# Performance work log

Hardware: AMD Instinct MI355X
Metric: run time of the kernel (lower is better)

The kernel has to match this reference:

```python
import jax, jax.numpy as jnp
import numpy as np

GAMMA = 0.1


def spmm(edge_index, edge_weight, feat, n_nodes):
    # y[dst] += w * feat[src]  -- sparse adjacency @ feat via gather/scatter
    src = edge_index[0]
    dst = edge_index[1]
    msgs = feat[src] * edge_weight[:, None]  # [E, d]
    return jax.ops.segment_sum(msgs, dst, num_segments=n_nodes)


def setup_inputs() -> dict:
    key = jax.random.key(0)
    ks = jax.random.split(key, 12)
    N, F, H, O = 50000, 500, 64, 16
    E, Ek = 1600000, 1000000
    x = jax.random.normal(ks[0], (N, F), dtype=jnp.float32)
    edge_index = jax.random.randint(ks[1], (2, E), 0, N, dtype=jnp.int32)
    edge_weight = jax.random.uniform(ks[2], (E,), dtype=jnp.float32)
    knn_edge_index = jax.random.randint(ks[3], (2, Ek), 0, N, dtype=jnp.int32)
    knn_edge_weight = jax.random.uniform(ks[4], (Ek,), dtype=jnp.float32)
    # glorot-ish scaled params
    W0 = jax.random.normal(ks[5], (F, H), dtype=jnp.float32) * (1.0 / np.sqrt(F))
    W1 = jax.random.normal(ks[6], (H, O), dtype=jnp.float32) * (1.0 / np.sqrt(H))
    score0 = jax.random.normal(ks[7], (F, 1), dtype=jnp.float32) * (1.0 / np.sqrt(F))
    score1 = jax.random.normal(ks[8], (H, 1), dtype=jnp.float32) * (1.0 / np.sqrt(H))
    Dk0 = jax.random.normal(ks[9], (F, 1), dtype=jnp.float32) * (1.0 / np.sqrt(F))
    Dk1 = jax.random.normal(ks[10], (H, 1), dtype=jnp.float32) * (1.0 / np.sqrt(H))
    z = jnp.zeros((1,), dtype=jnp.float32)
    return {
        "x": x, "edge_index": edge_index, "edge_weight": edge_weight,
        "knn_edge_index": knn_edge_index, "knn_edge_weight": knn_edge_weight,
        "W0": W0, "W1": W1,
        "score0": score0, "sbias0": z, "score1": score1, "sbias1": z,
        "Dk0": Dk0, "Dbias0": z, "Dk1": Dk1, "Dbias1": z,
    }


def reference(x, edge_index, edge_weight, knn_edge_index, knn_edge_weight,
              W0, W1, score0, sbias0, score1, sbias1,
              Dk0, Dbias0, Dk1, Dbias1):
    N = x.shape[0]
    layers = [(W0, score0, sbias0, Dk0, Dbias0),
              (W1, score1, sbias1, Dk1, Dbias1)]
    for W, sc, sb, dkw, dkb in layers:
        s = jax.nn.sigmoid(x @ sc + sb)          # [N, 1] gate
        Dk = x @ dkw + dkb                        # [N, 1] degree-like scale
        xW = x @ W                                # shared linear transform
        agg = spmm(edge_index, edge_weight, xW, N)        # GCNConv(x, adj)
        agg_knn = spmm(knn_edge_index, knn_edge_weight, xW, N)  # GCNConv(x, adj_knn)
        # acts are identity (acts=[None] and final act None); dropout off (eval)
        x = s * agg + (1.0 - s) * agg_knn + GAMMA * Dk * xW
    return x
```

## Files before the change

### kernel.cpp

```cpp
#include <hip/hip_runtime.h>
#include <math.h>

#define GAMMA 0.1f

typedef float f32x4 __attribute__((ext_vector_type(4)));
typedef short short4v __attribute__((ext_vector_type(4)));
typedef short short8 __attribute__((ext_vector_type(8)));

static __device__ __forceinline__ unsigned short f2bf(float f) {
  union { float f; unsigned u; } v; v.f = f;
  unsigned r = v.u + 0x7FFF + ((v.u >> 16) & 1);
  return (unsigned short)(r >> 16);
}
static __device__ __forceinline__ float bf2f(unsigned short b) {
  union { unsigned u; float f; } v; v.u = ((unsigned)b) << 16;
  return v.f;
}

__global__ __launch_bounds__(256) void build_bt3(
    const float* __restrict__ W, const float* __restrict__ sc,
    const float* __restrict__ dk, unsigned short* __restrict__ Bt3,
    int H, int Kact, int KPAD, int COLS) {
  int i = blockIdx.x * 256 + threadIdx.x;
  if (i >= COLS * KPAD) return;
  int c = i / KPAD;
  int k = i - c * KPAD;
  float v = 0.f;
  if (k < Kact) {
    if (c < H) v = W[(size_t)k * H + c];
    else if (c == H) v = sc[k];
    else if (c == H + 1) v = dk[k];
  }
  Bt3[(size_t)((k >> 3) * COLS + c) * 8 + (k & 7)] = f2bf(v);
}

__global__ __launch_bounds__(256) void zero_cnt(int* __restrict__ p, int n) {
  int i = blockIdx.x * 256 + threadIdx.x;
  if (i < n) p[i] = 0;
}

template <int CFRAGS, int OUTFRAGS, int COLS>
__global__ __launch_bounds__(256) void mfma_linear_l0(
    const float* __restrict__ A, const unsigned short* __restrict__ Bt3,
    const float* __restrict__ sb, const float* __restrict__ db,
    unsigned short* __restrict__ outW, float* __restrict__ s,
    float* __restrict__ Dk, int N, int Kact) {
  constexpr int KPAD = 512;
  constexpr int KSPLIT = 4, RPB = 16;
  constexpr int KS_PER = (KPAD / 32) / KSPLIT;
  constexpr int H = OUTFRAGS * 16;
  __shared__ unsigned short Ald[RPB * KPAD];
  __shared__ float red[(KSPLIT - 1) * 64 * CFRAGS * 4];

  const int t = threadIdx.x;
  const int rowBase = blockIdx.x * RPB;

#pragma unroll
  for (int it = 0; it < (RPB * KPAD) / (256 * 4); ++it) {
    int li = it * 1024 + t * 4;
    int row = li >> 9;
    int col = li & 511;
    int grow = rowBase + row;
    f32x4 v = (f32x4)0.f;
    if (grow < N && col < Kact)
      v = *(const f32x4*)(A + (size_t)grow * Kact + col);
    short4v b;
#pragma unroll
    for (int j = 0; j < 4; ++j) b[j] = (short)f2bf(v[j]);
    int byte = row * (KPAD * 2) + ((col * 2) ^ ((row & 7) << 4));
    *(short4v*)((char*)Ald + byte) = b;
  }
  __syncthreads();

  const int kslice = t >> 6;
  const int l = t & 63;
  const int kgrp = l >> 4;
  const int lc = l & 15;
  const int lrow = lc;
  const int rowD = rowBase + kgrp * 4;

  f32x4 acc[CFRAGS];
#pragma unroll
  for (int i = 0; i < CFRAGS; ++i) acc[i] = (f32x4)0.f;

  const int rbyte = lrow * (KPAD * 2);
  const int rswz = (lrow & 7) << 4;
#pragma unroll
  for (int kk = 0; kk < KS_PER; ++kk) {
    const int ks = kslice * KS_PER + kk;
    short8 av = *(const short8*)((char*)Ald +
                                 (rbyte + ((ks * 64 + kgrp * 16) ^ rswz)));
    const unsigned short* bbase =
        Bt3 + (size_t)((ks * 4 + kgrp) * COLS + lc) * 8;
#pragma unroll
    for (int fc = 0; fc < CFRAGS; ++fc) {
      short8 bv = *(const short8*)(bbase + fc * 128);
      acc[fc] = __builtin_amdgcn_mfma_f32_16x16x32_bf16(av, bv, acc[fc], 0, 0, 0);
    }
  }

  if (kslice > 0) {
    float* dst = red + ((kslice - 1) * 64 + l) * (CFRAGS * 4);
#pragma unroll
    for (int fc = 0; fc < CFRAGS; ++fc)
#pragma unroll
      for (int r = 0; r < 4; ++r) dst[fc * 4 + r] = acc[fc][r];
  }
  __syncthreads();
  if (kslice == 0) {
#pragma unroll
    for (int s2 = 1; s2 < KSPLIT; ++s2) {
      const float* src2 = red + ((s2 - 1) * 64 + l) * (CFRAGS * 4);
#pragma unroll
      for (int fc = 0; fc < CFRAGS; ++fc)
#pragma unroll
        for (int r = 0; r < 4; ++r) acc[fc][r] += src2[fc * 4 + r];
    }
#pragma unroll
    for (int fc = 0; fc < OUTFRAGS; ++fc) {
#pragma unroll
      for (int r = 0; r < 4; ++r) {
        int gr = rowD + r;
        if (gr < N) outW[(size_t)gr * H + fc * 16 + lc] = f2bf(acc[fc][r]);
      }
    }
    if (lc < 2) {
      f32x4 g = acc[CFRAGS - 1];
#pragma unroll
      for (int r = 0; r < 4; ++r) {
        int gr = rowD + r;
        if (gr < N) {
          if (lc == 0) s[gr] = 1.f / (1.f + expf(-(g[r] + sb[0])));
          else Dk[gr] = g[r] + db[0];
        }
      }
    }
  }
}

template <int KPAD, int CFRAGS, int OUTFRAGS, int COLS>
__global__ __launch_bounds__(256) void mfma_linear_bf(
    const unsigned short* __restrict__ Aptr, const unsigned short* __restrict__ Bt3,
    const float* __restrict__ sb, const float* __restrict__ db,
    unsigned short* __restrict__ outW, float* __restrict__ s,
    float* __restrict__ Dk, int N, int Kact) {
  constexpr int H = OUTFRAGS * 16;
  constexpr int KSPLIT = 2, RG = 2, RPB = 32;
  constexpr int KS_PER = (KPAD / 32) / KSPLIT;
  __shared__ float red[(KSPLIT - 1) * RG * 64 * CFRAGS * 4];

  const int w = threadIdx.x >> 6;
  const int rowgrp = w % RG;
  const int kslice = w / RG;
  const int l = threadIdx.x & 63;
  const int kgrp = l >> 4;
  const int lc = l & 15;
  const int rowA = blockIdx.x * RPB + rowgrp * 16 + lc;
  const int rowD = blockIdx.x * RPB + rowgrp * 16 + kgrp * 4;
  const int rowSafe = (rowA < N) ? rowA : 0;

  f32x4 acc[CFRAGS];
#pragma unroll
  for (int i = 0; i < CFRAGS; ++i) acc[i] = (f32x4)0.f;

#pragma unroll
  for (int kk = 0; kk < KS_PER; ++kk) {
    const int ks = kslice * KS_PER + kk;
    const int kb = ks * 32 + kgrp * 8;
    short8 av = *(const short8*)(Aptr + (size_t)rowSafe * Kact + kb);
    const unsigned short* bbase =
        Bt3 + (size_t)((ks * 4 + kgrp) * COLS + lc) * 8;
#pragma unroll
    for (int fc = 0; fc < CFRAGS; ++fc) {
      short8 bv = *(const short8*)(bbase + fc * 128);
      acc[fc] = __builtin_amdgcn_mfma_f32_16x16x32_bf16(av, bv, acc[fc], 0, 0, 0);
    }
  }

  if (kslice > 0) {
    float* dst = red + ((rowgrp)*64 + l) * (CFRAGS * 4);
#pragma unroll
    for (int fc = 0; fc < CFRAGS; ++fc)
#pragma unroll
      for (int r = 0; r < 4; ++r) dst[fc * 4 + r] = acc[fc][r];
  }
  __syncthreads();
  if (kslice == 0) {
    const float* src2 = red + ((rowgrp)*64 + l) * (CFRAGS * 4);
#pragma unroll
    for (int fc = 0; fc < CFRAGS; ++fc)
#pragma unroll
      for (int r = 0; r < 4; ++r) acc[fc][r] += src2[fc * 4 + r];

#pragma unroll
    for (int fc = 0; fc < OUTFRAGS; ++fc) {
#pragma unroll
      for (int r = 0; r < 4; ++r) {
        int gr = rowD + r;
        if (gr < N) outW[(size_t)gr * H + fc * 16 + lc] = f2bf(acc[fc][r]);
      }
    }
    if (lc < 2) {
      f32x4 g = acc[CFRAGS - 1];
#pragma unroll
      for (int r = 0; r < 4; ++r) {
        int gr = rowD + r;
        if (gr < N) {
          if (lc == 0) s[gr] = 1.f / (1.f + expf(-(g[r] + sb[0])));
          else Dk[gr] = g[r] + db[0];
        }
      }
    }
  }
}

#define BIN_CHUNK 8192

__global__ __launch_bounds__(512) void bucket_count2(
    const int* __restrict__ eiA, int EA, int* __restrict__ bcntA,
    const int* __restrict__ eiK, int EK, int* __restrict__ bcntK, int nchA) {
  const int* ei;
  int E, chunk;
  int* bcnt;
  if (blockIdx.x < nchA) { ei = eiA; E = EA; bcnt = bcntA; chunk = blockIdx.x; }
  else { ei = eiK; E = EK; bcnt = bcntK; chunk = blockIdx.x - nchA; }
  __shared__ int lc[256];
  if (threadIdx.x < 256) lc[threadIdx.x] = 0;
  __syncthreads();
  const int base = chunk * BIN_CHUNK;
  for (int k = threadIdx.x; k < BIN_CHUNK; k += 512) {
    int e = base + k;
    if (e < E) atomicAdd(&lc[ei[E + e] >> 8], 1);
  }
  __syncthreads();
  if (threadIdx.x < 256 && lc[threadIdx.x])
    atomicAdd(&bcnt[threadIdx.x], lc[threadIdx.x]);
}

__global__ __launch_bounds__(512) void bucket_scan2(
    int* __restrict__ bcntA, int* __restrict__ boffA, int* __restrict__ gcurA,
    int* __restrict__ bcntK, int* __restrict__ boffK, int* __restrict__ gcurK,
    int nb) {
  int* bcnt = blockIdx.x ? bcntK : bcntA;
  int* boff = blockIdx.x ? boffK : boffA;
  int* gcur = blockIdx.x ? gcurK : gcurA;
  __shared__ int sh[512];
  int t = threadIdx.x;
  int v = (t < nb) ? bcnt[t] : 0;
  sh[t] = v;
  __syncthreads();
  int acc = v;
  for (int off = 1; off < 512; off <<= 1) {
    int xx = (t >= off) ? sh[t - off] : 0;
    __syncthreads();
    acc += xx;
    sh[t] = acc;
    __syncthreads();
  }
  if (t < nb) {
    boff[t] = acc - v;
    gcur[t] = acc - v;
  }
  if (t == nb - 1) boff[nb] = acc;
}

__global__ __launch_bounds__(512) void bin_fill2(
    const int* __restrict__ eiA, const float* __restrict__ ewA, int EA,
    int* __restrict__ gcurA, int2* __restrict__ recA,
    const int* __restrict__ eiK, const float* __restrict__ ewK, int EK,
    int* __restrict__ gcurK, int2* __restrict__ recK, int nchA) {
  const int* ei;
  const float* ew;
  int E, chunk;
  int* gcur;
  int2* rec;
  if (blockIdx.x < nchA) {
    ei = eiA; ew = ewA; E = EA; gcur = gcurA; rec = recA; chunk = blockIdx.x;
  } else {
    ei = eiK; ew = ewK; E = EK; gcur = gcurK; rec = recK;
    chunk = blockIdx.x - nchA;
  }
  __shared__ int scnt[256];
  __shared__ int scur[256];
  if (threadIdx.x < 256) scnt[threadIdx.x] = 0;
  __syncthreads();
  const int base = chunk * BIN_CHUNK;
  for (int k = threadIdx.x; k < BIN_CHUNK; k += 512) {
    int e = base + k;
    if (e < E) atomicAdd(&scnt[ei[E + e] >> 8], 1);
  }
  __syncthreads();
  if (threadIdx.x < 256 && scnt[threadIdx.x])
    scur[threadIdx.x] = atomicAdd(&gcur[threadIdx.x], scnt[threadIdx.x]);
  __syncthreads();
  for (int k = threadIdx.x; k < BIN_CHUNK; k += 512) {
    int e = base + k;
    if (e < E) {
      int src = ei[e];
      int dst = ei[E + e];
      int pos = atomicAdd(&scur[dst >> 8], 1);
      rec[pos] = make_int2(((dst & 255) << 16) | src, __float_as_int(ew[e]));
    }
  }
}

__global__ __launch_bounds__(512) void tile_sort2(
    const int2* __restrict__ recRawA, const int* __restrict__ boffA,
    unsigned* __restrict__ recSA, int* __restrict__ rpA,
    const int2* __restrict__ recRawK, const int* __restrict__ boffK,
    unsigned* __restrict__ recSK, int* __restrict__ rpK, int N, int nb) {
  const int2* recRaw;
  const int* boff;
  unsigned* recS;
  int* rp;
  int tile;
  if (blockIdx.x < nb) {
    recRaw = recRawA; boff = boffA; recS = recSA; rp = rpA; tile = blockIdx.x;
  } else {
    recRaw = recRawK; boff = boffK; recS = recSK; rp = rpK;
    tile = blockIdx.x - nb;
  }
  __shared__ int cnt[256];
  __shared__ int sc[256];
  __shared__ int cur[256];
  const int lo = boff[tile], hi = boff[tile + 1];
  const int t = threadIdx.x;
  if (t < 256) cnt[t] = 0;
  __syncthreads();
  for (int j = lo + t; j < hi; j += 512)
    atomicAdd(&cnt[recRaw[j].x >> 16], 1);
  __syncthreads();
  if (t < 256) sc[t] = cnt[t];
  __syncthreads();
  for (int off = 1; off < 256; off <<= 1) {
    int v = 0;
    if (t < 256 && t >= off) v = sc[t - off];
    __syncthreads();
    if (t < 256) sc[t] += v;
    __syncthreads();
  }
  if (t < 256) {
    int excl = sc[t] - cnt[t];
    cur[t] = excl;
    int n = tile * 256 + t;
    if (n < N) rp[n] = lo + excl;
  }
  if (tile == nb - 1 && t == 0) rp[N] = hi;
  __syncthreads();
  for (int j = lo + t; j < hi; j += 512) {
    int2 r = recRaw[j];
    int pos = lo + atomicAdd(&cur[r.x >> 16], 1);
    recS[pos] = ((unsigned)f2bf(__int_as_float(r.y)) << 16) |
                (unsigned)(r.x & 0xFFFF);
  }
}

static __device__ __forceinline__ float gather64(
    const int* __restrict__ rp, const unsigned* __restrict__ rec,
    const unsigned short* __restrict__ feat, int n, int h) {
  int b = rp[n], e = rp[n + 1];
  float a[16];
#pragma unroll
  for (int u = 0; u < 16; ++u) a[u] = 0.f;
  int j = b;
  for (; j + 16 <= e; j += 16) {
#pragma unroll
    for (int u = 0; u < 16; ++u) {
      unsigned r = rec[j + u];
      a[u] += bf2f((unsigned short)(r >> 16)) *
              bf2f(feat[(size_t)(r & 0xFFFF) * 64 + h]);
    }
  }
  for (; j + 4 <= e; j += 4) {
#pragma unroll
    for (int u = 0; u < 4; ++u) {
      unsigned r = rec[j + u];
      a[u] += bf2f((unsigned short)(r >> 16)) *
              bf2f(feat[(size_t)(r & 0xFFFF) * 64 + h]);
    }
  }
  for (; j < e; ++j) {
    unsigned r = rec[j];
    a[0] += bf2f((unsigned short)(r >> 16)) *
            bf2f(feat[(size_t)(r & 0xFFFF) * 64 + h]);
  }
  float t0 = ((a[0] + a[1]) + (a[2] + a[3])) + ((a[4] + a[5]) + (a[6] + a[7]));
  float t1 = ((a[8] + a[9]) + (a[10] + a[11])) +
             ((a[12] + a[13]) + (a[14] + a[15]));
  return t0 + t1;
}

__global__ __launch_bounds__(256) void agg_combine64(
    const int* __restrict__ rpA, const unsigned* __restrict__ recA,
    const int* __restrict__ rpK, const unsigned* __restrict__ recK,
    const unsigned short* __restrict__ feat, const float* __restrict__ s,
    const float* __restrict__ Dk, unsigned short* __restrict__ outp, int N) {
  int n = __builtin_amdgcn_readfirstlane((blockIdx.x * 256 + threadIdx.x) >> 6);
  if (n >= N) return;
  int h = threadIdx.x & 63;
  float aA = gather64(rpA, recA, feat, n, h);
  float aK = gather64(rpK, recK, feat, n, h);
  float sv = s[n];
  float res = sv * aA + (1.f - sv) * aK +
              GAMMA * Dk[n] * bf2f(feat[(size_t)n * 64 + h]);
  outp[(size_t)n * 64 + h] = f2bf(res);
}

static __device__ __forceinline__ float gather16(
    const int* __restrict__ rp, const unsigned* __restrict__ rec,
    const unsigned short* __restrict__ feat, int n, int h) {
  int b = rp[n], e = rp[n + 1];
  float a0 = 0.f, a1 = 0.f, a2 = 0.f, a3 = 0.f;
  float a4 = 0.f, a5 = 0.f, a6 = 0.f, a7 = 0.f;
  int j = b;
  for (; j + 8 <= e; j += 8) {
    unsigned q0 = rec[j + 0];
    unsigned q1 = rec[j + 1];
    unsigned q2 = rec[j + 2];
    unsigned q3 = rec[j + 3];
    unsigned q4 = rec[j + 4];
    unsigned q5 = rec[j + 5];
    unsigned q6 = rec[j + 6];
    unsigned q7 = rec[j + 7];
    a0 += bf2f((unsigned short)(q0 >> 16)) *
          bf2f(feat[(size_t)(q0 & 0xFFFF) * 16 + h]);
    a1 += bf2f((unsigned short)(q1 >> 16)) *
          bf2f(feat[(size_t)(q1 & 0xFFFF) * 16 + h]);
    a2 += bf2f((unsigned short)(q2 >> 16)) *
          bf2f(feat[(size_t)(q2 & 0xFFFF) * 16 + h]);
    a3 += bf2f((unsigned short)(q3 >> 16)) *
          bf2f(feat[(size_t)(q3 & 0xFFFF) * 16 + h]);
    a4 += bf2f((unsigned short)(q4 >> 16)) *
          bf2f(feat[(size_t)(q4 & 0xFFFF) * 16 + h]);
    a5 += bf2f((unsigned short)(q5 >> 16)) *
          bf2f(feat[(size_t)(q5 & 0xFFFF) * 16 + h]);
    a6 += bf2f((unsigned short)(q6 >> 16)) *
          bf2f(feat[(size_t)(q6 & 0xFFFF) * 16 + h]);
    a7 += bf2f((unsigned short)(q7 >> 16)) *
          bf2f(feat[(size_t)(q7 & 0xFFFF) * 16 + h]);
  }
  for (; j < e; ++j) {
    unsigned q = rec[j];
    a0 += bf2f((unsigned short)(q >> 16)) *
          bf2f(feat[(size_t)(q & 0xFFFF) * 16 + h]);
  }
  return ((a0 + a1) + (a2 + a3)) + ((a4 + a5) + (a6 + a7));
}

__global__ __launch_bounds__(256) void agg_combine16(
    const int* __restrict__ rpA, const unsigned* __restrict__ recA,
    const int* __restrict__ rpK, const unsigned* __restrict__ recK,
    const unsigned short* __restrict__ feat, const float* __restrict__ s,
    const float* __restrict__ Dk, float* __restrict__ outp, int N) {
  int tid = blockIdx.x * 256 + threadIdx.x;
  int n = tid >> 4;
  int h = tid & 15;
  if (n >= N) return;
  float aA = gather16(rpA, recA, feat, n, h);
  float aK = gather16(rpK, recK, feat, n, h);
  float sv = s[n];
  float res = sv * aA + (1.f - sv) * aK +
              GAMMA * Dk[n] * bf2f(feat[(size_t)n * 16 + h]);
  outp[(size_t)n * 16 + h] = res;
}

extern "C" void kernel_launch(void* const* d_in, const int* in_sizes, int n_in,
                              void* d_out, int out_size, void* d_ws, size_t ws_size,
                              hipStream_t stream) {
  const float* x = (const float*)d_in[0];
  const int* edge_index = (const int*)d_in[1];
  const float* edge_weight = (const float*)d_in[2];
  const int* knn_edge_index = (const int*)d_in[3];
  const float* knn_edge_weight = (const float*)d_in[4];
  const float* W0 = (const float*)d_in[5];
  const float* W1 = (const float*)d_in[6];
  const float* score0 = (const float*)d_in[7];
  const float* sbias0 = (const float*)d_in[8];
  const float* score1 = (const float*)d_in[9];
  const float* sbias1 = (const float*)d_in[10];
  const float* Dk0 = (const float*)d_in[11];
  const float* Dbias0 = (const float*)d_in[12];
  const float* Dk1 = (const float*)d_in[13];
  const float* Dbias1 = (const float*)d_in[14];

  const int F = in_sizes[7];
  const int N = in_sizes[0] / F;
  const int E = in_sizes[2];
  const int Ek = in_sizes[4];
  (void)n_in; (void)ws_size; (void)out_size;

  const int nb = (N + 255) / 256;

  char* cur = (char*)d_ws;
  auto alloc = [&](size_t bytes) {
    char* p = cur;
    cur += (bytes + 255) & ~(size_t)255;
    return (void*)p;
  };
  float* sbuf = (float*)alloc((size_t)N * 4);
  float* dkbuf = (float*)alloc((size_t)N * 4);
  int* bcnt2 = (int*)alloc((size_t)2 * nb * 4);
  int* bcntA = bcnt2;
  int* bcntK = bcnt2 + nb;
  int* boffA = (int*)alloc((size_t)(nb + 1) * 4);
  int* boffK = (int*)alloc((size_t)(nb + 1) * 4);
  int* gcurA = (int*)alloc((size_t)nb * 4);
  int* gcurK = (int*)alloc((size_t)nb * 4);
  int* rpA = (int*)alloc((size_t)(N + 1) * 4);
  int* rpK = (int*)alloc((size_t)(N + 1) * 4);
  unsigned* recA = (unsigned*)alloc((size_t)E * 4);
  unsigned* recK = (unsigned*)alloc((size_t)Ek * 4);
  unsigned short* Bt0 = (unsigned short*)alloc((size_t)80 * 512 * 2);
  unsigned short* Bt1 = (unsigned short*)alloc((size_t)32 * 64 * 2);
  char* uni = (char*)alloc((size_t)(E + Ek) * 8);
  int2* recRawA = (int2*)uni;
  int2* recRawK = recRawA + E;
  unsigned short* xWb = (unsigned short*)uni;
  unsigned short* x1b = xWb + (size_t)N * 64;
  unsigned short* xW1b = x1b + (size_t)N * 64;

  build_bt3<<<(80 * 512 + 255) / 256, 256, 0, stream>>>(W0, score0, Dk0, Bt0,
                                                        64, F, 512, 80);
  build_bt3<<<(32 * 64 + 255) / 256, 256, 0, stream>>>(W1, score1, Dk1, Bt1,
                                                       16, 64, 64, 32);

  zero_cnt<<<(2 * nb + 255) / 256, 256, 0, stream>>>(bcnt2, 2 * nb);
  const int nchA = (E + BIN_CHUNK - 1) / BIN_CHUNK;
  const int nchK = (Ek + BIN_CHUNK - 1) / BIN_CHUNK;
  bucket_count2<<<nchA + nchK, 512, 0, stream>>>(edge_index, E, bcntA,
                                                 knn_edge_index, Ek, bcntK,
                                                 nchA);
  bucket_scan2<<<2, 512, 0, stream>>>(bcntA, boffA, gcurA, bcntK, boffK,
                                      gcurK, nb);
  bin_fill2<<<nchA + nchK, 512, 0, stream>>>(edge_index, edge_weight, E,
                                             gcurA, recRawA, knn_edge_index,
                                             knn_edge_weight, Ek, gcurK,
                                             recRawK, nchA);
  tile_sort2<<<2 * nb, 512, 0, stream>>>(recRawA, boffA, recA, rpA, recRawK,
                                         boffK, recK, rpK, N, nb);

  const int gemmBlocksL0 = (N + 15) / 16;
  const int gemmBlocksL1 = (N + 31) / 32;
  const int agg64Blocks = (int)(((size_t)N * 64 + 255) / 256);
  const int agg16Blocks = (int)(((size_t)N * 16 + 255) / 256);

  mfma_linear_l0<5, 4, 80><<<gemmBlocksL0, 256, 0, stream>>>(
      x, Bt0, sbias0, Dbias0, xWb, sbuf, dkbuf, N, F);
  agg_combine64<<<agg64Blocks, 256, 0, stream>>>(rpA, recA, rpK, recK, xWb,
                                                 sbuf, dkbuf, x1b, N);

  mfma_linear_bf<64, 2, 1, 32><<<gemmBlocksL1, 256, 0, stream>>>(
      x1b, Bt1, sbias1, Dbias1, xW1b, sbuf, dkbuf, N, 64);
  agg_combine16<<<agg16Blocks, 256, 0, stream>>>(rpA, recA, rpK, recK, xW1b,
                                                 sbuf, dkbuf, (float*)d_out, N);
}
```

Baseline: 174.1 us.

## Fuse layer-0 GEMM with edge bin-fill and merge setup kernels

Result: slower. 181.6 us (+4.3%).

```diff
diff --git a/kernel.cpp b/kernel.cpp
--- a/kernel.cpp
+++ b/kernel.cpp
@@ -17,204 +17,183 @@
   return v.f;
 }
 
-__global__ __launch_bounds__(256) void build_bt3(
-    const float* __restrict__ W, const float* __restrict__ sc,
-    const float* __restrict__ dk, unsigned short* __restrict__ Bt3,
-    int H, int Kact, int KPAD, int COLS) {
-  int i = blockIdx.x * 256 + threadIdx.x;
-  if (i >= COLS * KPAD) return;
-  int c = i / KPAD;
-  int k = i - c * KPAD;
-  float v = 0.f;
-  if (k < Kact) {
-    if (c < H) v = W[(size_t)k * H + c];
-    else if (c == H) v = sc[k];
-    else if (c == H + 1) v = dk[k];
-  }
-  Bt3[(size_t)((k >> 3) * COLS + c) * 8 + (k & 7)] = f2bf(v);
-}
-
-__global__ __launch_bounds__(256) void zero_cnt(int* __restrict__ p, int n) {
-  int i = blockIdx.x * 256 + threadIdx.x;
-  if (i < n) p[i] = 0;
-}
-
-template <int CFRAGS, int OUTFRAGS, int COLS>
-__global__ __launch_bounds__(256) void mfma_linear_l0(
+__global__ __launch_bounds__(256) void setup_fused(
+    int* __restrict__ bcnt2, int ncnt,
+    const float* __restrict__ W0, const float* __restrict__ sc0,
+    const float* __restrict__ dk0, unsigned short* __restrict__ Bt0, int F,
+    const float* __restrict__ W1, const float* __restrict__ sc1,
+    const float* __restrict__ dk1, unsigned short* __restrict__ Bt1) {
+  int b = blockIdx.x;
+  int t = threadIdx.x;
+  if (b < 2) {
+    int i = b * 256 + t;
+    if (i < ncnt) bcnt2[i] = 0;
+  } else if (b < 162) {
+    int i = (b - 2) * 256 + t;
+    int c = i >> 9;
+    int k = i & 511;
+    float v = 0.f;
+    if (k < F) {
+      if (c < 64) v = W0[(size_t)k * 64 + c];
+      else if (c == 64) v = sc0[k];
+      else if (c == 65) v = dk0[k];
+    }
+    Bt0[(size_t)((k >> 3) * 80 + c) * 8 + (k & 7)] = f2bf(v);
+  } else {
+    int i = (b - 162) * 256 + t;
+    int c = i >> 6;
+    int k = i & 63;
+    float v;
+    if (c < 16) v = W1[(size_t)k * 16 + c];
+    else if (c == 16) v = sc1[k];
+    else if (c == 17) v = dk1[k];
+    else v = 0.f;
+    Bt1[(size_t)((k >> 3) * 32 + c) * 8 + (k & 7)] = f2bf(v);
+  }
+}
+
+#define BIN_CHUNK 8192
+
+__global__ __launch_bounds__(256) void gemm_fill_fused(
     const float* __restrict__ A, const unsigned short* __restrict__ Bt3,
     const float* __restrict__ sb, const float* __restrict__ db,
     unsigned short* __restrict__ outW, float* __restrict__ s,
-    float* __restrict__ Dk, int N, int Kact) {
+    float* __restrict__ Dk, int N, int Kact, int gemmBlocks,
+    const int* __restrict__ eiA, const float* __restrict__ ewA, int EA,
+    int* __restrict__ gcurA, int2* __restrict__ recA,
+    const int* __restrict__ eiK, const float* __restrict__ ewK, int EK,
+    int* __restrict__ gcurK, int2* __restrict__ recK, int nchA) {
   constexpr int KPAD = 512;
   constexpr int KSPLIT = 4, RPB = 16;
   constexpr int KS_PER = (KPAD / 32) / KSPLIT;
+  constexpr int CFRAGS = 5, OUTFRAGS = 4, COLS = 80;
   constexpr int H = OUTFRAGS * 16;
   __shared__ unsigned short Ald[RPB * KPAD];
   __shared__ float red[(KSPLIT - 1) * 64 * CFRAGS * 4];
+  __shared__ int scnt[256];
+  __shared__ int scur[256];
 
   const int t = threadIdx.x;
-  const int rowBase = blockIdx.x * RPB;
-
-#pragma unroll
-  for (int it = 0; it < (RPB * KPAD) / (256 * 4); ++it) {
-    int li = it * 1024 + t * 4;
-    int row = li >> 9;
-    int col = li & 511;
-    int grow = rowBase + row;
-    f32x4 v = (f32x4)0.f;
-    if (grow < N && col < Kact)
-      v = *(const f32x4*)(A + (size_t)grow * Kact + col);
-    short4v b;
-#pragma unroll
-    for (int j = 0; j < 4; ++j) b[j] = (short)f2bf(v[j]);
-    int byte = row * (KPAD * 2) + ((col * 2) ^ ((row & 7) << 4));
-    *(short4v*)((char*)Ald + byte) = b;
-  }
-  __syncthreads();
-
-  const int kslice = t >> 6;
-  const int l = t & 63;
-  const int kgrp = l >> 4;
-  const int lc = l & 15;
-  const int lrow = lc;
-  const int rowD = rowBase + kgrp * 4;
-
-  f32x4 acc[CFRAGS];
-#pragma unroll
-  for (int i = 0; i < CFRAGS; ++i) acc[i] = (f32x4)0.f;
-
-  const int rbyte = lrow * (KPAD * 2);
-  const int rswz = (lrow & 7) << 4;
-#pragma unroll
-  for (int kk = 0; kk < KS_PER; ++kk) {
-    const int ks = kslice * KS_PER + kk;
-    short8 av = *(const short8*)((char*)Ald +
-                                 (rbyte + ((ks * 64 + kgrp * 16) ^ rswz)));
-    const unsigned short* bbase =
-        Bt3 + (size_t)((ks * 4 + kgrp) * COLS + lc) * 8;
-#pragma unroll
-    for (int fc = 0; fc < CFRAGS; ++fc) {
-      short8 bv = *(const short8*)(bbase + fc * 128);
-      acc[fc] = __builtin_amdgcn_mfma_f32_16x16x32_bf16(av, bv, acc[fc], 0, 0, 0);
-    }
-  }
-
-  if (kslice > 0) {
-    float* dst = red + ((kslice - 1) * 64 + l) * (CFRAGS * 4);
-#pragma unroll
-    for (int fc = 0; fc < CFRAGS; ++fc)
-#pragma unroll
-      for (int r = 0; r < 4; ++r) dst[fc * 4 + r] = acc[fc][r];
-  }
-  __syncthreads();
-  if (kslice == 0) {
-#pragma unroll
-    for (int s2 = 1; s2 < KSPLIT; ++s2) {
-      const float* src2 = red + ((s2 - 1) * 64 + l) * (CFRAGS * 4);
+
+  if (blockIdx.x < gemmBlocks) {
+    const int rowBase = blockIdx.x * RPB;
+
+#pragma unroll
+    for (int it = 0; it < (RPB * KPAD) / (256 * 4); ++it) {
+      int li = it * 1024 + t * 4;
+      int row = li >> 9;
+      int col = li & 511;
+      int grow = rowBase + row;
+      f32x4 v = (f32x4)0.f;
+      if (grow < N && col < Kact)
+        v = *(const f32x4*)(A + (size_t)grow * Kact + col);
+      short4v bb;
+#pragma unroll
+      for (int j = 0; j < 4; ++j) bb[j] = (short)f2bf(v[j]);
+      int byte = row * (KPAD * 2) + ((col * 2) ^ ((row & 7) << 4));
+      *(short4v*)((char*)Ald + byte) = bb;
+    }
+    __syncthreads();
+
+    const int kslice = t >> 6;
+    const int l = t & 63;
+    const int kgrp = l >> 4;
+    const int lc = l & 15;
+    const int lrow = lc;
+    const int rowD = rowBase + kgrp * 4;
+
+    f32x4 acc[CFRAGS];
+#pragma unroll
+    for (int i = 0; i < CFRAGS; ++i) acc[i] = (f32x4)0.f;
+
+    const int rbyte = lrow * (KPAD * 2);
+    const int rswz = (lrow & 7) << 4;
+#pragma unroll
+    for (int kk = 0; kk < KS_PER; ++kk) {
+      const int ks = kslice * KS_PER + kk;
+      short8 av = *(const short8*)((char*)Ald +
+                                   (rbyte + ((ks * 64 + kgrp * 16) ^ rswz)));
+      const unsigned short* bbase =
+          Bt3 + (size_t)((ks * 4 + kgrp) * COLS + lc) * 8;
+#pragma unroll
+      for (int fc = 0; fc < CFRAGS; ++fc) {
+        short8 bv = *(const short8*)(bbase + fc * 128);
+        acc[fc] =
+            __builtin_amdgcn_mfma_f32_16x16x32_bf16(av, bv, acc[fc], 0, 0, 0);
+      }
+    }
+
+    if (kslice > 0) {
+      float* dst = red + ((kslice - 1) * 64 + l) * (CFRAGS * 4);
 #pragma unroll
       for (int fc = 0; fc < CFRAGS; ++fc)
 #pragma unroll
-        for (int r = 0; r < 4; ++r) acc[fc][r] += src2[fc * 4 + r];
-    }
-#pragma unroll
-    for (int fc = 0; fc < OUTFRAGS; ++fc) {
-#pragma unroll
-      for (int r = 0; r < 4; ++r) {
-        int gr = rowD + r;
-        if (gr < N) outW[(size_t)gr * H + fc * 16 + lc] = f2bf(acc[fc][r]);
-      }
-    }
-    if (lc < 2) {
-      f32x4 g = acc[CFRAGS - 1];
-#pragma unroll
-      for (int r = 0; r < 4; ++r) {
-        int gr = rowD + r;
-        if (gr < N) {
-          if (lc == 0) s[gr] = 1.f / (1.f + expf(-(g[r] + sb[0])));
-          else Dk[gr] = g[r] + db[0];
+        for (int r = 0; r < 4; ++r) dst[fc * 4 + r] = acc[fc][r];
+    }
+    __syncthreads();
+    if (kslice == 0) {
+#pragma unroll
+      for (int s2 = 1; s2 < KSPLIT; ++s2) {
+        const float* src2 = red + ((s2 - 1) * 64 + l) * (CFRAGS * 4);
+#pragma unroll
+        for (int fc = 0; fc < CFRAGS; ++fc)
+#pragma unroll
+          for (int r = 0; r < 4; ++r) acc[fc][r] += src2[fc * 4 + r];
+      }
+#pragma unroll
+      for (int fc = 0; fc < OUTFRAGS; ++fc) {
+#pragma unroll
+        for (int r = 0; r < 4; ++r) {
+          int gr = rowD + r;
+          if (gr < N) outW[(size_t)gr * H + fc * 16 + lc] = f2bf(acc[fc][r]);
         }
       }
-    }
-  }
-}
-
-template <int KPAD, int CFRAGS, int OUTFRAGS, int COLS>
-__global__ __launch_bounds__(256) void mfma_linear_bf(
-    const unsigned short* __restrict__ Aptr, const unsigned short* __restrict__ Bt3,
-    const float* __restrict__ sb, const float* __restrict__ db,
-    unsigned short* __restrict__ outW, float* __restrict__ s,
-    float* __restrict__ Dk, int N, int Kact) {
-  constexpr int H = OUTFRAGS * 16;
-  constexpr int KSPLIT = 2, RG = 2, RPB = 32;
-  constexpr int KS_PER = (KPAD / 32) / KSPLIT;
-  __shared__ float red[(KSPLIT - 1) * RG * 64 * CFRAGS * 4];
-
-  const int w = threadIdx.x >> 6;
-  const int rowgrp = w % RG;
-  const int kslice = w / RG;
-  const int l = threadIdx.x & 63;
-  const int kgrp = l >> 4;
-  const int lc = l & 15;
-  const int rowA = blockIdx.x * RPB + rowgrp * 16 + lc;
-  const int rowD = blockIdx.x * RPB + rowgrp * 16 + kgrp * 4;
-  const int rowSafe = (rowA < N) ? rowA : 0;
-
-  f32x4 acc[CFRAGS];
-#pragma unroll
-  for (int i = 0; i < CFRAGS; ++i) acc[i] = (f32x4)0.f;
-
-#pragma unroll
-  for (int kk = 0; kk < KS_PER; ++kk) {
-    const int ks = kslice * KS_PER + kk;
-    const int kb = ks * 32 + kgrp * 8;
-    short8 av = *(const short8*)(Aptr + (size_t)rowSafe * Kact + kb);
-    const unsigned short* bbase =
-        Bt3 + (size_t)((ks * 4 + kgrp) * COLS + lc) * 8;
-#pragma unroll
-    for (int fc = 0; fc < CFRAGS; ++fc) {
-      short8 bv = *(const short8*)(bbase + fc * 128);
-      acc[fc] = __builtin_amdgcn_mfma_f32_16x16x32_bf16(av, bv, acc[fc], 0, 0, 0);
-    }
-  }
-
-  if (kslice > 0) {
-    float* dst = red + ((rowgrp)*64 + l) * (CFRAGS * 4);
-#pragma unroll
-    for (int fc = 0; fc < CFRAGS; ++fc)
-#pragma unroll
-      for (int r = 0; r < 4; ++r) dst[fc * 4 + r] = acc[fc][r];
-  }
-  __syncthreads();
-  if (kslice == 0) {
-    const float* src2 = red + ((rowgrp)*64 + l) * (CFRAGS * 4);
-#pragma unroll
-    for (int fc = 0; fc < CFRAGS; ++fc)
-#pragma unroll
-      for (int r = 0; r < 4; ++r) acc[fc][r] += src2[fc * 4 + r];
-
-#pragma unroll
-    for (int fc = 0; fc < OUTFRAGS; ++fc) {
-#pragma unroll
-      for (int r = 0; r < 4; ++r) {
-        int gr = rowD + r;
-        if (gr < N) outW[(size_t)gr * H + fc * 16 + lc] = f2bf(acc[fc][r]);
-      }
-    }
-    if (lc < 2) {
-      f32x4 g = acc[CFRAGS - 1];
-#pragma unroll
-      for (int r = 0; r < 4; ++r) {
-        int gr = rowD + r;
-        if (gr < N) {
-          if (lc == 0) s[gr] = 1.f / (1.f + expf(-(g[r] + sb[0])));
-          else Dk[gr] = g[r] + db[0];
+      if (lc < 2) {
+        f32x4 g = acc[CFRAGS - 1];
+#pragma unroll
+        for (int r = 0; r < 4; ++r) {
+          int gr = rowD + r;
+          if (gr < N) {
+            if (lc == 0) s[gr] = 1.f / (1.f + expf(-(g[r] + sb[0])));
+            else Dk[gr] = g[r] + db[0];
+          }
         }
       }
     }
-  }
-}
-
-#define BIN_CHUNK 8192
+  } else {
+    int fb = blockIdx.x - gemmBlocks;
+    const int* ei;
+    const float* ew;
+    int E, chunk;
+    int* gcur;
+    int2* rec;
+    if (fb < nchA) {
+      ei = eiA; ew = ewA; E = EA; gcur = gcurA; rec = recA; chunk = fb;
+    } else {
+      ei = eiK; ew = ewK; E = EK; gcur = gcurK; rec = recK;
+      chunk = fb - nchA;
+    }
+    scnt[t] = 0;
+    __syncthreads();
+    const int base = chunk * BIN_CHUNK;
+    for (int k = t; k < BIN_CHUNK; k += 256) {
+      int e = base + k;
+      if (e < E) atomicAdd(&scnt[ei[E + e] >> 8], 1);
+    }
+    __syncthreads();
+    if (scnt[t]) scur[t] = atomicAdd(&gcur[t], scnt[t]);
+    __syncthreads();
+    for (int k = t; k < BIN_CHUNK; k += 256) {
+      int e = base + k;
+      if (e < E) {
+        int src = ei[e];
+        int dst = ei[E + e];
+        int pos = atomicAdd(&scur[dst >> 8], 1);
+        rec[pos] = make_int2(((dst & 255) << 16) | src, __float_as_int(ew[e]));
+      }
+    }
+  }
+}
 
 __global__ __launch_bounds__(512) void bucket_count2(
     const int* __restrict__ eiA, int EA, int* __restrict__ bcntA,
@@ -262,46 +241,6 @@
     gcur[t] = acc - v;
   }
   if (t == nb - 1) boff[nb] = acc;
-}
-
-__global__ __launch_bounds__(512) void bin_fill2(
-    const int* __restrict__ eiA, const float* __restrict__ ewA, int EA,
-    int* __restrict__ gcurA, int2* __restrict__ recA,
-    const int* __restrict__ eiK, const float* __restrict__ ewK, int EK,
-    int* __restrict__ gcurK, int2* __restrict__ recK, int nchA) {
-  const int* ei;
-  const float* ew;
-  int E, chunk;
-  int* gcur;
-  int2* rec;
-  if (blockIdx.x < nchA) {
-    ei = eiA; ew = ewA; E = EA; gcur = gcurA; rec = recA; chunk = blockIdx.x;
-  } else {
-    ei = eiK; ew = ewK; E = EK; gcur = gcurK; rec = recK;
-    chunk = blockIdx.x - nchA;
-  }
-  __shared__ int scnt[256];
-  __shared__ int scur[256];
-  if (threadIdx.x < 256) scnt[threadIdx.x] = 0;
-  __syncthreads();
-  const int base = chunk * BIN_CHUNK;
-  for (int k = threadIdx.x; k < BIN_CHUNK; k += 512) {
-    int e = base + k;
-    if (e < E) atomicAdd(&scnt[ei[E + e] >> 8], 1);
-  }
-  __syncthreads();
-  if (threadIdx.x < 256 && scnt[threadIdx.x])
-    scur[threadIdx.x] = atomicAdd(&gcur[threadIdx.x], scnt[threadIdx.x]);
-  __syncthreads();
-  for (int k = threadIdx.x; k < BIN_CHUNK; k += 512) {
-    int e = base + k;
-    if (e < E) {
-      int src = ei[e];
-      int dst = ei[E + e];
-      int pos = atomicAdd(&scur[dst >> 8], 1);
-      rec[pos] = make_int2(((dst & 255) << 16) | src, __float_as_int(ew[e]));
-    }
-  }
 }
 
 __global__ __launch_bounds__(512) void tile_sort2(
@@ -352,6 +291,82 @@
     int pos = lo + atomicAdd(&cur[r.x >> 16], 1);
     recS[pos] = ((unsigned)f2bf(__int_as_float(r.y)) << 16) |
                 (unsigned)(r.x & 0xFFFF);
+  }
+}
+
+template <int KPAD, int CFRAGS, int OUTFRAGS, int COLS>
+__global__ __launch_bounds__(256) void mfma_linear_bf(
+    const unsigned short* __restrict__ Aptr, const unsigned short* __restrict__ Bt3,
+    const float* __restrict__ sb, const float* __restrict__ db,
+    unsigned short* __restrict__ outW, float* __restrict__ s,
+    float* __restrict__ Dk, int N, int Kact) {
+  constexpr int H = OUTFRAGS * 16;
+  constexpr int KSPLIT = 2, RG = 2, RPB = 32;
+  constexpr int KS_PER = (KPAD / 32) / KSPLIT;
+  __shared__ float red[(KSPLIT - 1) * RG * 64 * CFRAGS * 4];
+
+  const int w = threadIdx.x >> 6;
+  const int rowgrp = w % RG;
+  const int kslice = w / RG;
+  const int l = threadIdx.x & 63;
+  const int kgrp = l >> 4;
+  const int lc = l & 15;
+  const int rowA = blockIdx.x * RPB + rowgrp * 16 + lc;
+  const int rowD = blockIdx.x * RPB + rowgrp * 16 + kgrp * 4;
+  const int rowSafe = (rowA < N) ? rowA : 0;
+
+  f32x4 acc[CFRAGS];
+#pragma unroll
+  for (int i = 0; i < CFRAGS; ++i) acc[i] = (f32x4)0.f;
+
+#pragma unroll
+  for (int kk = 0; kk < KS_PER; ++kk) {
+    const int ks = kslice * KS_PER + kk;
+    const int kb = ks * 32 + kgrp * 8;
+    short8 av = *(const short8*)(Aptr + (size_t)rowSafe * Kact + kb);
+    const unsigned short* bbase =
+        Bt3 + (size_t)((ks * 4 + kgrp) * COLS + lc) * 8;
+#pragma unroll
+    for (int fc = 0; fc < CFRAGS; ++fc) {
+      short8 bv = *(const short8*)(bbase + fc * 128);
+      acc[fc] = __builtin_amdgcn_mfma_f32_16x16x32_bf16(av, bv, acc[fc], 0, 0, 0);
+    }
+  }
+
+  if (kslice > 0) {
+    float* dst = red + ((rowgrp)*64 + l) * (CFRAGS * 4);
+#pragma unroll
+    for (int fc = 0; fc < CFRAGS; ++fc)
+#pragma unroll
+      for (int r = 0; r < 4; ++r) dst[fc * 4 + r] = acc[fc][r];
+  }
+  __syncthreads();
+  if (kslice == 0) {
+    const float* src2 = red + ((rowgrp)*64 + l) * (CFRAGS * 4);
+#pragma unroll
+    for (int fc = 0; fc < CFRAGS; ++fc)
+#pragma unroll
+      for (int r = 0; r < 4; ++r) acc[fc][r] += src2[fc * 4 + r];
+
+#pragma unroll
+    for (int fc = 0; fc < OUTFRAGS; ++fc) {
+#pragma unroll
+      for (int r = 0; r < 4; ++r) {
+        int gr = rowD + r;
+        if (gr < N) outW[(size_t)gr * H + fc * 16 + lc] = f2bf(acc[fc][r]);
+      }
+    }
+    if (lc < 2) {
+      f32x4 g = acc[CFRAGS - 1];
+#pragma unroll
+      for (int r = 0; r < 4; ++r) {
+        int gr = rowD + r;
+        if (gr < N) {
+          if (lc == 0) s[gr] = 1.f / (1.f + expf(-(g[r] + sb[0])));
+          else Dk[gr] = g[r] + db[0];
+        }
+      }
+    }
   }
 }
 
@@ -512,43 +527,34 @@
   unsigned* recK = (unsigned*)alloc((size_t)Ek * 4);
   unsigned short* Bt0 = (unsigned short*)alloc((size_t)80 * 512 * 2);
   unsigned short* Bt1 = (unsigned short*)alloc((size_t)32 * 64 * 2);
-  char* uni = (char*)alloc((size_t)(E + Ek) * 8);
-  int2* recRawA = (int2*)uni;
-  int2* recRawK = recRawA + E;
-  unsigned short* xWb = (unsigned short*)uni;
-  unsigned short* x1b = xWb + (size_t)N * 64;
-  unsigned short* xW1b = x1b + (size_t)N * 64;
-
-  build_bt3<<<(80 * 512 + 255) / 256, 256, 0, stream>>>(W0, score0, Dk0, Bt0,
-                                                        64, F, 512, 80);
-  build_bt3<<<(32 * 64 + 255) / 256, 256, 0, stream>>>(W1, score1, Dk1, Bt1,
-                                                       16, 64, 64, 32);
-
-  zero_cnt<<<(2 * nb + 255) / 256, 256, 0, stream>>>(bcnt2, 2 * nb);
+  int2* recRawA = (int2*)alloc((size_t)E * 8);
+  int2* recRawK = (int2*)alloc((size_t)Ek * 8);
+  unsigned short* xWb = (unsigned short*)alloc((size_t)N * 64 * 2);
+  unsigned short* x1b = (unsigned short*)alloc((size_t)N * 64 * 2);
+  unsigned short* xW1b = (unsigned short*)alloc((size_t)N * 16 * 2);
+
   const int nchA = (E + BIN_CHUNK - 1) / BIN_CHUNK;
   const int nchK = (Ek + BIN_CHUNK - 1) / BIN_CHUNK;
+  const int gemmBlocksL0 = (N + 15) / 16;
+  const int gemmBlocksL1 = (N + 31) / 32;
+  const int agg64Blocks = (int)(((size_t)N * 64 + 255) / 256);
+  const int agg16Blocks = (int)(((size_t)N * 16 + 255) / 256);
+
+  setup_fused<<<170, 256, 0, stream>>>(bcnt2, 2 * nb, W0, score0, Dk0, Bt0, F,
+                                       W1, score1, Dk1, Bt1);
   bucket_count2<<<nchA + nchK, 512, 0, stream>>>(edge_index, E, bcntA,
                                                  knn_edge_index, Ek, bcntK,
                                                  nchA);
   bucket_scan2<<<2, 512, 0, stream>>>(bcntA, boffA, gcurA, bcntK, boffK,
                                       gcurK, nb);
-  bin_fill2<<<nchA + nchK, 512, 0, stream>>>(edge_index, edge_weight, E,
-                                             gcurA, recRawA, knn_edge_index,
-                                             knn_edge_weight, Ek, gcurK,
-                                             recRawK, nchA);
+  gemm_fill_fused<<<gemmBlocksL0 + nchA + nchK, 256, 0, stream>>>(
+      x, Bt0, sbias0, Dbias0, xWb, sbuf, dkbuf, N, F, gemmBlocksL0,
+      edge_index, edge_weight, E, gcurA, recRawA, knn_edge_index,
+      knn_edge_weight, Ek, gcurK, recRawK, nchA);
   tile_sort2<<<2 * nb, 512, 0, stream>>>(recRawA, boffA, recA, rpA, recRawK,
                                          boffK, recK, rpK, N, nb);
-
-  const int gemmBlocksL0 = (N + 15) / 16;
-  const int gemmBlocksL1 = (N + 31) / 32;
-  const int agg64Blocks = (int)(((size_t)N * 64 + 255) / 256);
-  const int agg16Blocks = (int)(((size_t)N * 16 + 255) / 256);
-
-  mfma_linear_l0<5, 4, 80><<<gemmBlocksL0, 256, 0, stream>>>(
-      x, Bt0, sbias0, Dbias0, xWb, sbuf, dkbuf, N, F);
   agg_combine64<<<agg64Blocks, 256, 0, stream>>>(rpA, recA, rpK, recK, xWb,
                                                  sbuf, dkbuf, x1b, N);
-
   mfma_linear_bf<64, 2, 1, 32><<<gemmBlocksL1, 256, 0, stream>>>(
       x1b, Bt1, sbias1, Dbias1, xW1b, sbuf, dkbuf, N, 64);
   agg_combine16<<<agg16Blocks, 256, 0, stream>>>(rpA, recA, rpK, recK, xW1b,
```
